# Kernel tuning notes

Hardware: AMD Instinct MI355X
Metric: run time of the kernel (lower is better)

Reference implementation:

```python
import jax, jax.numpy as jnp
import numpy as np
import math

B, L = 512, 50
NW, A, N, H = 50000, 512, 8, 256
EPS = 1e-5


def setup_inputs() -> dict:
    key = jax.random.key(0)
    ks = jax.random.split(key, 32)
    std = 1.0 / math.sqrt(H)
    nrm = lambda k, shape: jax.random.normal(k, shape, dtype=jnp.float32) * std
    inp = {}
    inp["inp_seq"] = jax.random.randint(ks[0], (B, L), 0, NW)
    inp["topic_mat"] = jax.random.normal(ks[1], (NW, A), dtype=jnp.float32)
    inp["dr_w"] = nrm(ks[2], (A, H))
    inp["dr_b"] = nrm(ks[3], (H,))
    inp["w1_w"] = nrm(ks[4], (N, H, H))
    inp["w1_b"] = nrm(ks[5], (N, H))
    inp["w2_w"] = nrm(ks[6], (N, H, H))
    inp["w2_b"] = nrm(ks[7], (N, H))
    inp["v_w"] = nrm(ks[8], (N, H))
    inp["lin0_w"] = nrm(ks[9], (2 * N * H, H))
    inp["lin0_b"] = nrm(ks[10], (H,))
    for i, base in zip((1, 2, 3), (11, 15, 19)):
        inp[f"l{i}_w"] = nrm(ks[base], (H, H))
        inp[f"l{i}_b"] = nrm(ks[base + 1], (H,))
        inp[f"g{i}"] = nrm(ks[base + 2], (H,))
        inp[f"be{i}"] = nrm(ks[base + 3], (H,))
    inp["out_w"] = nrm(ks[23], (H, NW - 1))
    return inp


def _bn(x, g, b):
    # BatchNorm1d, training mode: batch statistics (biased variance)
    m = jnp.mean(x, axis=0)
    v = jnp.var(x, axis=0)
    return (x - m) * jax.lax.rsqrt(v + EPS) * g + b


def reference(inp_seq, topic_mat, dr_w, dr_b, w1_w, w1_b, w2_w, w2_b, v_w,
              lin0_w, lin0_b, l1_w, l1_b, g1, be1, l2_w, l2_b, g2, be2,
              l3_w, l3_b, g3, be3, out_w):
    fea = jax.nn.relu(topic_mat[inp_seq] @ dr_w + dr_b)          # [B,L,H]
    mask = (inp_seq > 0).astype(fea.dtype)                        # [B,L]
    ht = fea[:, -1, :]                                            # [B,H]
    # all N heads batched: additive attention
    q1 = jnp.einsum('bh,nhd->bnd', ht, w1_w) + w1_b               # [B,N,H]
    q2 = jnp.einsum('blh,nhd->bnld', fea, w2_w) + w2_b[None, :, None, :]  # [B,N,L,H]
    alpha = jnp.einsum('bnlh,nh->bnl', jax.nn.sigmoid(q1[:, :, None, :] + q2), v_w)
    a = jnp.einsum('bnl,blh->bnh', alpha * mask[:, None, :], fea)  # [B,N,H]
    ht_rep = jnp.broadcast_to(ht[:, None, :], (a.shape[0], N, H))
    c_final = jnp.concatenate([a, ht_rep], axis=-1).reshape(a.shape[0], 2 * N * H)
    c = jax.nn.relu(c_final @ lin0_w + lin0_b)                    # [B,H]
    h = jax.nn.relu(_bn(c @ l1_w + l1_b, g1, be1))
    h = jax.nn.relu(_bn(h @ l2_w + l2_b, g2, be2))
    h = jax.nn.relu(_bn(h @ l3_w + l3_b, g3, be3))
    return (h + c) @ out_w                                        # [B, NW-1]
```

## Files before the change

kernel.cpp:

```cpp
#include <hip/hip_runtime.h>

typedef __attribute__((ext_vector_type(4))) float f32x4;
typedef __attribute__((ext_vector_type(4))) unsigned int u32x4;
typedef __attribute__((ext_vector_type(8))) short short8;
typedef __attribute__((ext_vector_type(4))) unsigned short u16x4;

#define DEV static __device__ __forceinline__

DEV unsigned short f2bf(float f) {
  union { float f; unsigned u; } v; v.f = f;
  unsigned r = v.u + 0x7fffu + ((v.u >> 16) & 1u);
  return (unsigned short)(r >> 16);
}
DEV float bf2f(unsigned short s) {
  union { unsigned u; float f; } v; v.u = ((unsigned)s) << 16;
  return v.f;
}

constexpr int KS = 32;
constexpr int LR = 40;

template<int BM, int BN, int TH, int WY, int WX, bool ABF16, bool GATHER,
         int BMODE, bool RELU, int OUTM, bool SPLITK, bool SWZ>
__global__ __launch_bounds__(TH)
void gemm_k(const void* __restrict__ Av, int lda, int rmul, int radd,
            const int* __restrict__ gidx,
            const void* __restrict__ Bp, int ldb,
            const float* __restrict__ bias,
            float* __restrict__ Cf, unsigned short* __restrict__ Cb, int ldc,
            int M, int N, int K)
{
  constexpr int WM = BM / WY, WN = BN / WX, FM = WM / 16, FN = WN / 16;
  __shared__ unsigned short As[2][BM][LR];
  __shared__ unsigned short Bs[2][BN][LR];
  const int tid = threadIdx.x;
  const int lane = tid & 63;
  const int wid = tid >> 6;
  const int wy = wid / WX, wx = wid % WX;
  int bx = blockIdx.x, by = blockIdx.y;
  if constexpr (SWZ) {
    const int gx = gridDim.x, total = gx * gridDim.y;
    const int bid = by * gx + bx;
    const int q = total >> 3, r = total & 7;
    const int xcd = bid & 7, idx = bid >> 3;
    const int j = (xcd < r ? xcd * (q + 1) : r * (q + 1) + (xcd - r) * q) + idx;
    bx = j % gx; by = j / gx;
  }
  const long m0 = (long)bx * BM;
  const int n0 = by * BN;
  const int kbeg = SPLITK ? blockIdx.z * K : 0;
  if constexpr (SPLITK) Cf += (long)blockIdx.z * M * ldc;

  f32x4 acc[FM][FN];
#pragma unroll
  for (int i = 0; i < FM; ++i)
#pragma unroll
    for (int j = 0; j < FN; ++j) acc[i][j] = (f32x4)0.f;

  const int nsteps = K / KS;

  auto stageA = [&](int ks, int buf) {
    const int k0 = kbeg + ks * KS;
    if constexpr (!ABF16) {
      const float* A = (const float*)Av;
#pragma unroll
      for (int p = 0; p < BM / (TH / 8); ++p) {
        const int r = p * (TH / 8) + (tid >> 3);
        const int kq = tid & 7;
        long ar = GATHER ? (long)gidx[m0 + r] : ((m0 + r) * (long)rmul + radd);
        f32x4 v = *(const f32x4*)(A + ar * lda + k0 + kq * 4);
        u16x4 o;
        o[0] = f2bf(v[0]); o[1] = f2bf(v[1]); o[2] = f2bf(v[2]); o[3] = f2bf(v[3]);
        *(u16x4*)(&As[buf][r][kq * 4]) = o;
      }
    } else {
      const unsigned short* A = (const unsigned short*)Av;
#pragma unroll
      for (int p = 0; p < BM / (TH / 4); ++p) {
        const int r = p * (TH / 4) + (tid >> 2);
        const int cq = tid & 3;
        long ar = (m0 + r) * (long)rmul + radd;
        u32x4 v = *(const u32x4*)(A + ar * lda + k0 + cq * 8);
        *(u32x4*)(&As[buf][r][cq * 8]) = v;
      }
    }
  };

  auto stageB = [&](int ks, int buf) {
    if constexpr (BMODE == 0) {
      const float* B = (const float*)Bp;
      const int k0 = kbeg + ks * KS;
      constexpr int NC = BN / 4;
#pragma unroll
      for (int p = 0; p < (KS * NC) / TH; ++p) {
        const int n4 = tid % NC;
        const int k = p * (TH / NC) + tid / NC;
        const int c0 = n0 + n4 * 4;
        f32x4 v;
        if (c0 + 3 < N) {
          v = *(const f32x4*)(B + (long)(k0 + k) * ldb + c0);
        } else {
#pragma unroll
          for (int e = 0; e < 4; ++e)
            v[e] = (c0 + e < N) ? B[(long)(k0 + k) * ldb + c0 + e] : 0.f;
        }
        Bs[buf][n4 * 4 + 0][k] = f2bf(v[0]);
        Bs[buf][n4 * 4 + 1][k] = f2bf(v[1]);
        Bs[buf][n4 * 4 + 2][k] = f2bf(v[2]);
        Bs[buf][n4 * 4 + 3][k] = f2bf(v[3]);
      }
    } else {
      const unsigned short* B = (const unsigned short*)Bp;
      const int ksg = (kbeg / KS) + ks;
#pragma unroll
      for (int p = 0; p < (BN * 4) / TH; ++p) {
        const int cc = p * (TH / 4) + (tid >> 2);
        const int q = tid & 3;
        u32x4 v = *(const u32x4*)(B + ((long)ksg * ldb + n0 + cc) * 32 + q * 8);
        *(u32x4*)(&Bs[buf][cc][q * 8]) = v;
      }
    }
  };

  stageA(0, 0); stageB(0, 0);

  for (int ks = 0; ks < nsteps; ++ks) {
    __syncthreads();
    if (ks + 1 < nsteps) { stageA(ks + 1, (ks + 1) & 1); stageB(ks + 1, (ks + 1) & 1); }
    const int buf = ks & 1;
    short8 ar[FM], br[FN];
#pragma unroll
    for (int fm = 0; fm < FM; ++fm)
      ar[fm] = *(const short8*)(&As[buf][wy * WM + fm * 16 + (lane & 15)][(lane >> 4) * 8]);
#pragma unroll
    for (int fn = 0; fn < FN; ++fn)
      br[fn] = *(const short8*)(&Bs[buf][wx * WN + fn * 16 + (lane & 15)][(lane >> 4) * 8]);
#pragma unroll
    for (int fm = 0; fm < FM; ++fm)
#pragma unroll
      for (int fn = 0; fn < FN; ++fn)
        acc[fm][fn] = __builtin_amdgcn_mfma_f32_16x16x32_bf16(ar[fm], br[fn], acc[fm][fn], 0, 0, 0);
  }

#pragma unroll
  for (int fm = 0; fm < FM; ++fm) {
    const long row0 = m0 + wy * WM + fm * 16 + ((lane >> 4) << 2);
#pragma unroll
    for (int fn = 0; fn < FN; ++fn) {
      const int col = n0 + wx * WN + fn * 16 + (lane & 15);
      if (col >= N) continue;
      const float bv = bias ? bias[col] : 0.f;
#pragma unroll
      for (int j = 0; j < 4; ++j) {
        float v = acc[fm][fn][j] + bv;
        if constexpr (RELU) v = fmaxf(v, 0.f);
        const long r = row0 + j;
        if constexpr (OUTM & 1) Cf[r * ldc + col] = v;
        if constexpr (OUTM & 2) Cb[r * ldc + col] = f2bf(v);
      }
    }
  }
}

__global__ __launch_bounds__(256)
void packB_k(const float* __restrict__ src, unsigned short* __restrict__ dst,
             int Nsrc, int Ndst)
{
  const int t = blockIdx.x * 256 + threadIdx.x;
  const int ks = t / Ndst, n = t - ks * Ndst;
  unsigned short buf[32];
#pragma unroll
  for (int kk = 0; kk < 32; ++kk)
    buf[kk] = (n < Nsrc) ? f2bf(src[(long)(ks * 32 + kk) * Nsrc + n]) : (unsigned short)0;
#pragma unroll
  for (int q = 0; q < 4; ++q)
    *(u32x4*)(dst + ((long)ks * Ndst + n) * 32 + q * 8) = *(const u32x4*)(buf + q * 8);
}

__global__ __launch_bounds__(256)
void alpha_k(const unsigned short* __restrict__ fea,
             const unsigned short* __restrict__ w2t,
             const float* __restrict__ q1buf,
             const float* __restrict__ vw,
             float* __restrict__ alpha)
{
  __shared__ unsigned short As[2][64][LR];
  __shared__ unsigned short Bs[2][256][LR];
  __shared__ float vws[256];
  __shared__ float red[4][64];
  const int tid = threadIdx.x;
  const int lane = tid & 63;
  const int w = tid >> 6;
  const int m0 = blockIdx.x * 64;
  const int n = blockIdx.y;

  vws[tid] = vw[n * 256 + tid];

  f32x4 acc[4][4];
#pragma unroll
  for (int i = 0; i < 4; ++i)
#pragma unroll
    for (int j = 0; j < 4; ++j) acc[i][j] = (f32x4)0.f;

  auto stageA = [&](int ks, int buf) {
    const int k0 = ks * KS;
    const int r = tid >> 2, cq = tid & 3;
    u32x4 v = *(const u32x4*)(fea + (long)(m0 + r) * 256 + k0 + cq * 8);
    *(u32x4*)(&As[buf][r][cq * 8]) = v;
  };
  auto stageB = [&](int ks, int buf) {
    const int k0 = ks * KS;
#pragma unroll
    for (int p = 0; p < 4; ++p) {
      const int r = p * 64 + (tid >> 2), cq = tid & 3;
      u32x4 v = *(const u32x4*)(w2t + ((long)(n * 256 + r)) * 256 + k0 + cq * 8);
      *(u32x4*)(&Bs[buf][r][cq * 8]) = v;
    }
  };

  stageA(0, 0); stageB(0, 0);
  for (int ks = 0; ks < 8; ++ks) {
    __syncthreads();
    if (ks < 7) { stageA(ks + 1, (ks + 1) & 1); stageB(ks + 1, (ks + 1) & 1); }
    const int buf = ks & 1;
    short8 ar[4], br[4];
#pragma unroll
    for (int fm = 0; fm < 4; ++fm)
      ar[fm] = *(const short8*)(&As[buf][fm * 16 + (lane & 15)][(lane >> 4) * 8]);
#pragma unroll
    for (int fn = 0; fn < 4; ++fn)
      br[fn] = *(const short8*)(&Bs[buf][w * 64 + fn * 16 + (lane & 15)][(lane >> 4) * 8]);
#pragma unroll
    for (int fm = 0; fm < 4; ++fm)
#pragma unroll
      for (int fn = 0; fn < 4; ++fn)
        acc[fm][fn] = __builtin_amdgcn_mfma_f32_16x16x32_bf16(ar[fm], br[fn], acc[fm][fn], 0, 0, 0);
  }

  const int g = lane >> 4, c = lane & 15;
  float part[4][4];
#pragma unroll
  for (int fm = 0; fm < 4; ++fm) {
#pragma unroll
    for (int j = 0; j < 4; ++j) {
      const int m = m0 + fm * 16 + g * 4 + j;
      const int b = m / 50;
      float p = 0.f;
#pragma unroll
      for (int fn = 0; fn < 4; ++fn) {
        const int col = w * 64 + fn * 16 + c;
        const float q = acc[fm][fn][j] + q1buf[(long)b * 2048 + n * 256 + col];
        const float s = 1.f / (1.f + __expf(-q));
        p += s * vws[col];
      }
      part[fm][j] = p;
    }
  }
#pragma unroll
  for (int fm = 0; fm < 4; ++fm)
#pragma unroll
    for (int j = 0; j < 4; ++j)
#pragma unroll
      for (int off = 1; off < 16; off <<= 1)
        part[fm][j] += __shfl_xor(part[fm][j], off);
  if (c == 0) {
#pragma unroll
    for (int fm = 0; fm < 4; ++fm)
#pragma unroll
      for (int j = 0; j < 4; ++j)
        red[w][fm * 16 + g * 4 + j] = part[fm][j];
  }
  __syncthreads();
  if (tid < 64) {
    const float s = red[0][tid] + red[1][tid] + red[2][tid] + red[3][tid];
    const int m = m0 + tid;
    const int b = m / 50, l = m - b * 50;
    alpha[((long)b * 8 + n) * 50 + l] = s;
  }
}

__global__ __launch_bounds__(256)
void cfinal_k(const unsigned short* __restrict__ fea,
              const float* __restrict__ alpha,
              const int* __restrict__ seq,
              unsigned short* __restrict__ cfin)
{
  __shared__ unsigned short feas[50][256];
  __shared__ float al[8][50];
  const int b = blockIdx.x, t = threadIdx.x;
#pragma unroll 1
  for (int l = 0; l < 50; ++l)
    feas[l][t] = fea[((long)b * 50 + l) * 256 + t];
  for (int i = t; i < 400; i += 256) {
    const int nn = i / 50, l = i - nn * 50;
    const float mk = (seq[b * 50 + l] > 0) ? 1.f : 0.f;
    al[nn][l] = alpha[((long)b * 8 + nn) * 50 + l] * mk;
  }
  __syncthreads();
#pragma unroll 1
  for (int nn = 0; nn < 8; ++nn) {
    float acc = 0.f;
#pragma unroll
    for (int l = 0; l < 50; ++l) acc += al[nn][l] * bf2f(feas[l][t]);
    cfin[(long)b * 2304 + nn * 256 + t] = f2bf(acc);
  }
  cfin[(long)b * 2304 + 2048 + t] = feas[49][t];
}

__global__ __launch_bounds__(256)
void lin0red_k(const float* __restrict__ part, const float* __restrict__ bias,
               float* __restrict__ cf, unsigned short* __restrict__ cb)
{
  const int e = blockIdx.x * 256 + threadIdx.x;
  float s = bias[e & 255];
#pragma unroll
  for (int z = 0; z < 8; ++z) s += part[z * 131072 + e];
  s = fmaxf(s, 0.f);
  cf[e] = s;
  cb[e] = f2bf(s);
}

template<bool LAST>
__global__ __launch_bounds__(256)
void bn_k(const float* __restrict__ y, const float* __restrict__ g,
          const float* __restrict__ be, const float* __restrict__ cres,
          unsigned short* __restrict__ out)
{
  const int t = threadIdx.x;
  const int col = blockIdx.x * 8 + (t & 7);
  const int rg = t >> 3;
  float v[16];
  float s = 0.f, q = 0.f;
#pragma unroll
  for (int i = 0; i < 16; ++i) {
    const int off = (rg + i * 32) * 256 + col;
    float x = y[off] + y[131072 + off] + y[262144 + off] + y[393216 + off];
    v[i] = x;
    s += x; q += x * x;
  }
  for (int off = 8; off < 64; off <<= 1) { s += __shfl_xor(s, off); q += __shfl_xor(q, off); }
  __shared__ float ps[4][8], pq[4][8], mm[8], rr[8];
  if ((t & 63) < 8) { ps[t >> 6][t & 7] = s; pq[t >> 6][t & 7] = q; }
  __syncthreads();
  if (t < 8) {
    const float S = ps[0][t] + ps[1][t] + ps[2][t] + ps[3][t];
    const float Q = pq[0][t] + pq[1][t] + pq[2][t] + pq[3][t];
    const float m = S * (1.f / 512.f);
    const float var = Q * (1.f / 512.f) - m * m;
    mm[t] = m;
    rr[t] = rsqrtf(var + 1e-5f);
  }
  __syncthreads();
  const float m = mm[t & 7], r = rr[t & 7], gg = g[col], bb = be[col];
#pragma unroll
  for (int i = 0; i < 16; ++i) {
    float h = (v[i] - m) * r * gg + bb;
    h = fmaxf(h, 0.f);
    if constexpr (LAST) h += cres[(rg + i * 32) * 256 + col];
    out[(rg + i * 32) * 256 + col] = f2bf(h);
  }
}

__global__ __launch_bounds__(256)
void prepack_k(const float* __restrict__ w1w, const float* __restrict__ w1b,
               const float* __restrict__ w2w, const float* __restrict__ w2b,
               float* __restrict__ w1t, float* __restrict__ bias12,
               unsigned short* __restrict__ w2t)
{
  const int tid = blockIdx.x * 256 + threadIdx.x;
  if (tid < 524288) {
    const int nn = tid >> 16, rem = tid & 65535, h = rem >> 8, d = rem & 255;
    w1t[h * 2048 + nn * 256 + d] = w1w[tid];
    w2t[((long)(nn * 256 + d)) * 256 + h] = f2bf(w2w[tid]);
  }
  if (tid < 2048) bias12[tid] = w1b[tid] + w2b[tid];
}

__global__ __launch_bounds__(256)
void prepack2_k(const float* __restrict__ lin0w, float* __restrict__ wcat)
{
  const int e = blockIdx.x * 256 + threadIdx.x;
  const int h2 = e >> 8, d = e & 255;
  float v;
  if (h2 < 2048) {
    const int n = h2 >> 8, h = h2 & 255;
    v = lin0w[((n * 512 + h) << 8) + d];
  } else {
    const int h = h2 - 2048;
    v = 0.f;
#pragma unroll
    for (int n = 0; n < 8; ++n) v += lin0w[((n * 512 + 256 + h) << 8) + d];
  }
  wcat[e] = v;
}

extern "C" void kernel_launch(void* const* d_in, const int* in_sizes, int n_in,
                              void* d_out, int out_size, void* d_ws, size_t ws_size,
                              hipStream_t stream)
{
  const int*   seq    = (const int*)  d_in[0];
  const float* topic  = (const float*)d_in[1];
  const float* dr_w   = (const float*)d_in[2];
  const float* dr_b   = (const float*)d_in[3];
  const float* w1_w   = (const float*)d_in[4];
  const float* w1_b   = (const float*)d_in[5];
  const float* w2_w   = (const float*)d_in[6];
  const float* w2_b   = (const float*)d_in[7];
  const float* v_w    = (const float*)d_in[8];
  const float* lin0_w = (const float*)d_in[9];
  const float* lin0_b = (const float*)d_in[10];
  const float* l1_w   = (const float*)d_in[11];
  const float* g1     = (const float*)d_in[13];
  const float* be1    = (const float*)d_in[14];
  const float* l2_w   = (const float*)d_in[15];
  const float* g2     = (const float*)d_in[17];
  const float* be2    = (const float*)d_in[18];
  const float* l3_w   = (const float*)d_in[19];
  const float* g3     = (const float*)d_in[21];
  const float* be3    = (const float*)d_in[22];
  const float* out_w  = (const float*)d_in[23];
  float* outp = (float*)d_out;

  char* ws = (char*)d_ws;
  size_t off = 0;
  auto alloc = [&](size_t bytes) -> void* {
    void* p = ws + off;
    off += (bytes + 255) & ~(size_t)255;
    return p;
  };
  unsigned short* fea    = (unsigned short*)alloc(25600ull * 256 * 2);
  unsigned short* w2t    = (unsigned short*)alloc(8ull * 256 * 256 * 2);
  float* w1t             = (float*)alloc(256ull * 2048 * 4);
  float* bias12          = (float*)alloc(2048ull * 4);
  float* q1buf           = (float*)alloc(512ull * 2048 * 4);
  float* alphab          = (float*)alloc(512ull * 8 * 50 * 4);
  unsigned short* cfin   = (unsigned short*)alloc(512ull * 2304 * 2);
  float* wcat            = (float*)alloc(2304ull * 256 * 4);
  float* part            = (float*)alloc(8ull * 512 * 256 * 4);
  float* c_f32           = (float*)alloc(512ull * 256 * 4);
  unsigned short* c_bf   = (unsigned short*)alloc(512ull * 256 * 2);
  unsigned short* h_bf   = (unsigned short*)alloc(512ull * 256 * 2);
  unsigned short* hc_bf  = (unsigned short*)alloc(512ull * 256 * 2);
  unsigned short* drwp   = (unsigned short*)alloc(16ull * 256 * 32 * 2);
  unsigned short* wpad   = (unsigned short*)alloc(8ull * 50048 * 32 * 2);

  hipLaunchKernelGGL(prepack_k, dim3(2048), dim3(256), 0, stream,
                     w1_w, w1_b, w2_w, w2_b, w1t, bias12, w2t);
  hipLaunchKernelGGL(prepack2_k, dim3(2304), dim3(256), 0, stream, lin0_w, wcat);
  hipLaunchKernelGGL(packB_k, dim3(16), dim3(256), 0, stream, dr_w, drwp, 256, 256);
  hipLaunchKernelGGL(packB_k, dim3(1564), dim3(256), 0, stream, out_w, wpad, 49999, 50048);

  hipLaunchKernelGGL((gemm_k<64,256,256,1,4, false,true, 1, true, 2, false,false>),
                     dim3(400, 1), dim3(256), 0, stream,
                     (const void*)topic, 512, 1, 0, seq, (const void*)drwp, 256, dr_b,
                     (float*)nullptr, fea, 256, 25600, 256, 512);

  hipLaunchKernelGGL((gemm_k<64,64,256,2,2, true,false, 0, false, 1, false,false>),
                     dim3(8, 32), dim3(256), 0, stream,
                     (const void*)fea, 256, 50, 49, (const int*)nullptr,
                     (const void*)w1t, 2048, bias12,
                     q1buf, (unsigned short*)nullptr, 2048, 512, 2048, 256);

  hipLaunchKernelGGL(alpha_k, dim3(400, 8), dim3(256), 0, stream,
                     fea, w2t, q1buf, v_w, alphab);

  hipLaunchKernelGGL(cfinal_k, dim3(512), dim3(256), 0, stream, fea, alphab, seq, cfin);

  hipLaunchKernelGGL((gemm_k<64,64,256,2,2, true,false, 0, false, 1, true,false>),
                     dim3(8, 4, 8), dim3(256), 0, stream,
                     (const void*)cfin, 2304, 1, 0, (const int*)nullptr,
                     (const void*)wcat, 256, (const float*)nullptr,
                     part, (unsigned short*)nullptr, 256, 512, 256, 288);
  hipLaunchKernelGGL(lin0red_k, dim3(512), dim3(256), 0, stream, part, lin0_b, c_f32, c_bf);

  hipLaunchKernelGGL((gemm_k<64,64,256,2,2, true,false, 0, false, 1, true,false>),
                     dim3(8, 4, 4), dim3(256), 0, stream,
                     (const void*)c_bf, 256, 1, 0, (const int*)nullptr,
                     (const void*)l1_w, 256, (const float*)nullptr,
                     part, (unsigned short*)nullptr, 256, 512, 256, 64);
  hipLaunchKernelGGL((bn_k<false>), dim3(32), dim3(256), 0, stream,
                     part, g1, be1, (const float*)nullptr, h_bf);

  hipLaunchKernelGGL((gemm_k<64,64,256,2,2, true,false, 0, false, 1, true,false>),
                     dim3(8, 4, 4), dim3(256), 0, stream,
                     (const void*)h_bf, 256, 1, 0, (const int*)nullptr,
                     (const void*)l2_w, 256, (const float*)nullptr,
                     part, (unsigned short*)nullptr, 256, 512, 256, 64);
  hipLaunchKernelGGL((bn_k<false>), dim3(32), dim3(256), 0, stream,
                     part, g2, be2, (const float*)nullptr, h_bf);

  hipLaunchKernelGGL((gemm_k<64,64,256,2,2, true,false, 0, false, 1, true,false>),
                     dim3(8, 4, 4), dim3(256), 0, stream,
                     (const void*)h_bf, 256, 1, 0, (const int*)nullptr,
                     (const void*)l3_w, 256, (const float*)nullptr,
                     part, (unsigned short*)nullptr, 256, 512, 256, 64);
  hipLaunchKernelGGL((bn_k<true>), dim3(32), dim3(256), 0, stream,
                     part, g3, be3, c_f32, hc_bf);

  hipLaunchKernelGGL((gemm_k<128,128,256,2,2, true,false, 1, false, 1, false,true>),
                     dim3(4, 391), dim3(256), 0, stream,
                     (const void*)hc_bf, 256, 1, 0, (const int*)nullptr,
                     (const void*)wpad, 50048, (const float*)nullptr,
                     outp, (unsigned short*)nullptr, 49999, 512, 49999, 256);

  (void)in_sizes; (void)n_in; (void)out_size; (void)ws_size;
}
```

Before: 509.4 us.

## Split alpha kernel over hidden-column halves and stage q1 in shared memory

The attention-score kernel now splits the 256 hidden columns across two grid z-slices, each block computing a 64x128 tile with a 2x2 warp layout. Each slice writes a partial alpha to its own buffer, and the context kernel sums the two partials. q1 values for the block's rows are preloaded into shared memory instead of being read from global memory per element, and the sigmoid uses a fast reciprocal. This doubles block count and lowers per-block register and LDS use for occupancy, at the cost of reloading the fea A-tile twice and extra alpha traffic.

```diff
diff --git a/kernel.cpp b/kernel.cpp
--- a/kernel.cpp
+++ b/kernel.cpp
@@ -185,20 +185,30 @@
              float* __restrict__ alpha)
 {
   __shared__ unsigned short As[2][64][LR];
-  __shared__ unsigned short Bs[2][256][LR];
-  __shared__ float vws[256];
-  __shared__ float red[4][64];
+  __shared__ unsigned short Bs[2][128][LR];
+  __shared__ float vws[128];
+  __shared__ float q1s[3][128];
+  __shared__ float red[2][64];
   const int tid = threadIdx.x;
   const int lane = tid & 63;
   const int w = tid >> 6;
+  const int wy = w >> 1, wx = w & 1;
   const int m0 = blockIdx.x * 64;
   const int n = blockIdx.y;
-
-  vws[tid] = vw[n * 256 + tid];
-
-  f32x4 acc[4][4];
-#pragma unroll
-  for (int i = 0; i < 4; ++i)
+  const int z = blockIdx.z;
+  const int c0g = z * 128;
+  const int b0 = m0 / 50;
+
+  if (tid < 128) vws[tid] = vw[n * 256 + c0g + tid];
+  for (int i = tid; i < 384; i += 256) {
+    const int bi = i >> 7, cc = i & 127;
+    const int bb = min(b0 + bi, 511);
+    q1s[bi][cc] = q1buf[(long)bb * 2048 + n * 256 + c0g + cc];
+  }
+
+  f32x4 acc[2][4];
+#pragma unroll
+  for (int i = 0; i < 2; ++i)
 #pragma unroll
     for (int j = 0; j < 4; ++j) acc[i][j] = (f32x4)0.f;
 
@@ -211,9 +221,9 @@
   auto stageB = [&](int ks, int buf) {
     const int k0 = ks * KS;
 #pragma unroll
-    for (int p = 0; p < 4; ++p) {
+    for (int p = 0; p < 2; ++p) {
       const int r = p * 64 + (tid >> 2), cq = tid & 3;
-      u32x4 v = *(const u32x4*)(w2t + ((long)(n * 256 + r)) * 256 + k0 + cq * 8);
+      u32x4 v = *(const u32x4*)(w2t + ((long)(n * 256 + c0g + r)) * 256 + k0 + cq * 8);
       *(u32x4*)(&Bs[buf][r][cq * 8]) = v;
     }
   };
@@ -223,41 +233,41 @@
     __syncthreads();
     if (ks < 7) { stageA(ks + 1, (ks + 1) & 1); stageB(ks + 1, (ks + 1) & 1); }
     const int buf = ks & 1;
-    short8 ar[4], br[4];
-#pragma unroll
-    for (int fm = 0; fm < 4; ++fm)
-      ar[fm] = *(const short8*)(&As[buf][fm * 16 + (lane & 15)][(lane >> 4) * 8]);
+    short8 ar[2], br[4];
+#pragma unroll
+    for (int fm = 0; fm < 2; ++fm)
+      ar[fm] = *(const short8*)(&As[buf][wy * 32 + fm * 16 + (lane & 15)][(lane >> 4) * 8]);
 #pragma unroll
     for (int fn = 0; fn < 4; ++fn)
-      br[fn] = *(const short8*)(&Bs[buf][w * 64 + fn * 16 + (lane & 15)][(lane >> 4) * 8]);
-#pragma unroll
-    for (int fm = 0; fm < 4; ++fm)
+      br[fn] = *(const short8*)(&Bs[buf][wx * 64 + fn * 16 + (lane & 15)][(lane >> 4) * 8]);
+#pragma unroll
+    for (int fm = 0; fm < 2; ++fm)
 #pragma unroll
       for (int fn = 0; fn < 4; ++fn)
         acc[fm][fn] = __builtin_amdgcn_mfma_f32_16x16x32_bf16(ar[fm], br[fn], acc[fm][fn], 0, 0, 0);
   }
 
   const int g = lane >> 4, c = lane & 15;
-  float part[4][4];
-#pragma unroll
-  for (int fm = 0; fm < 4; ++fm) {
+  float part[2][4];
+#pragma unroll
+  for (int fm = 0; fm < 2; ++fm) {
 #pragma unroll
     for (int j = 0; j < 4; ++j) {
-      const int m = m0 + fm * 16 + g * 4 + j;
-      const int b = m / 50;
+      const int m = m0 + wy * 32 + fm * 16 + g * 4 + j;
+      const int bi = m / 50 - b0;
       float p = 0.f;
 #pragma unroll
       for (int fn = 0; fn < 4; ++fn) {
-        const int col = w * 64 + fn * 16 + c;
-        const float q = acc[fm][fn][j] + q1buf[(long)b * 2048 + n * 256 + col];
-        const float s = 1.f / (1.f + __expf(-q));
-        p += s * vws[col];
+        const int colL = wx * 64 + fn * 16 + c;
+        const float q = acc[fm][fn][j] + q1s[bi][colL];
+        const float e = __expf(-q);
+        p += vws[colL] * __builtin_amdgcn_rcpf(1.f + e);
       }
       part[fm][j] = p;
     }
   }
 #pragma unroll
-  for (int fm = 0; fm < 4; ++fm)
+  for (int fm = 0; fm < 2; ++fm)
 #pragma unroll
     for (int j = 0; j < 4; ++j)
 #pragma unroll
@@ -265,17 +275,17 @@
         part[fm][j] += __shfl_xor(part[fm][j], off);
   if (c == 0) {
 #pragma unroll
-    for (int fm = 0; fm < 4; ++fm)
+    for (int fm = 0; fm < 2; ++fm)
 #pragma unroll
       for (int j = 0; j < 4; ++j)
-        red[w][fm * 16 + g * 4 + j] = part[fm][j];
+        red[wx][wy * 32 + fm * 16 + g * 4 + j] = part[fm][j];
   }
   __syncthreads();
   if (tid < 64) {
-    const float s = red[0][tid] + red[1][tid] + red[2][tid] + red[3][tid];
+    const float s = red[0][tid] + red[1][tid];
     const int m = m0 + tid;
     const int b = m / 50, l = m - b * 50;
-    alpha[((long)b * 8 + n) * 50 + l] = s;
+    alpha[(((long)z * 512 + b) * 8 + n) * 50 + l] = s;
   }
 }
 
@@ -294,7 +304,8 @@
   for (int i = t; i < 400; i += 256) {
     const int nn = i / 50, l = i - nn * 50;
     const float mk = (seq[b * 50 + l] > 0) ? 1.f : 0.f;
-    al[nn][l] = alpha[((long)b * 8 + nn) * 50 + l] * mk;
+    const long idx = ((long)b * 8 + nn) * 50 + l;
+    al[nn][l] = (alpha[idx] + alpha[204800 + idx]) * mk;
   }
   __syncthreads();
 #pragma unroll 1
@@ -433,7 +444,7 @@
   float* w1t             = (float*)alloc(256ull * 2048 * 4);
   float* bias12          = (float*)alloc(2048ull * 4);
   float* q1buf           = (float*)alloc(512ull * 2048 * 4);
-  float* alphab          = (float*)alloc(512ull * 8 * 50 * 4);
+  float* alphab          = (float*)alloc(2ull * 512 * 8 * 50 * 4);
   unsigned short* cfin   = (unsigned short*)alloc(512ull * 2304 * 2);
   float* wcat            = (float*)alloc(2304ull * 256 * 4);
   float* part            = (float*)alloc(8ull * 512 * 256 * 4);
@@ -461,7 +472,7 @@
                      (const void*)w1t, 2048, bias12,
                      q1buf, (unsigned short*)nullptr, 2048, 512, 2048, 256);
 
-  hipLaunchKernelGGL(alpha_k, dim3(400, 8), dim3(256), 0, stream,
+  hipLaunchKernelGGL(alpha_k, dim3(400, 8, 2), dim3(256), 0, stream,
                      fea, w2t, q1buf, v_w, alphab);
 
   hipLaunchKernelGGL(cfinal_k, dim3(512), dim3(256), 0, stream, fea, alphab, seq, cfin);
```

New measurement: 479.9 us. 1.06x faster.
